# Kernel tuning notes

Hardware: AMD Instinct MI355X
Metric: run time of the kernel (lower is better)

Reference implementation:

```python
import jax, jax.numpy as jnp
import numpy as np

B, H, L, D = 8, 16, 1024, 64


def setup_inputs() -> dict:
    key = jax.random.key(0)
    kq, kk, kv, kb, km = jax.random.split(key, 5)
    q = jax.random.normal(kq, (B, H, L, D), dtype=jnp.float32)
    k = jax.random.normal(kk, (B, H, L, D), dtype=jnp.float32)
    v = jax.random.normal(kv, (B, H, L, D), dtype=jnp.float32)
    # relative-position bias, broadcast over batch
    bias = jax.random.normal(kb, (1, H, L, L), dtype=jnp.float32)
    # variable-length padding mask: each sequence has length in [L//2, L]
    lengths = jax.random.randint(km, (B,), L // 2, L + 1)
    mask = jnp.arange(L)[None, :] < lengths[:, None]  # [B, L] bool
    return {"q": q, "k": k, "v": v, "mask": mask, "bias": bias}


def reference(q, k, v, mask, bias):
    # dots: [b h m n]; NOTE: source computes self.scale but never applies it
    dots = jnp.einsum('bhmd,bhnd->bhmn', q, k) + bias
    # mask[:, None, None, :] & mask[:, None, :, None]
    m2 = mask[:, None, None, :] & mask[:, None, :, None]  # [b 1 m n]
    neg = jnp.finfo(dots.dtype).min
    probs = jax.nn.softmax(jnp.where(m2, dots, neg), axis=-1)
    probs = jnp.where(m2, probs, jnp.zeros((), dtype=probs.dtype))  # XSoftmax zeroing
    # dropout is identity in eval mode
    context = jnp.einsum('bhmn,bhnd->bhmd', probs, v)
    b, h, m, d = context.shape
    return context.transpose(0, 2, 1, 3).reshape(b, m, h * d)  # [b m (h d)]
```

## Files before the change

kernel.cpp:

```cpp
#include <hip/hip_runtime.h>
#include <hip/hip_bf16.h>

#define B_ 8
#define H_ 16
#define L_ 1024
#define D_ 64

typedef __attribute__((ext_vector_type(8))) short short8;
typedef __attribute__((ext_vector_type(4))) short short4v;
typedef __attribute__((ext_vector_type(4))) float floatx4;

__device__ inline short bf16s(float f) {
    union { float f; unsigned u; } un; un.f = f;
    unsigned u = un.u;
    u += 0x7FFFu + ((u >> 16) & 1u);
    return (short)(u >> 16);
}
__device__ inline float bf16f(unsigned short u) {
    union { unsigned u; float f; } un; un.u = ((unsigned)u) << 16;
    return un.f;
}

__device__ inline floatx4 mfma16(short8 a, short8 b, floatx4 c) {
    return __builtin_amdgcn_mfma_f32_16x16x32_bf16(a, b, c, 0, 0, 0);
}

#define KSTR 72
#define VSTR 40
#define PSTR 40
#define KPL (32 * KSTR)
#define VPL (64 * VSTR)
#define PPL (16 * PSTR)

__launch_bounds__(256, 4)
__global__ void prep_kernel(const float* __restrict__ k,
                            const float* __restrict__ v,
                            unsigned short* __restrict__ khi,
                            unsigned short* __restrict__ klo,
                            unsigned short* __restrict__ vth) {
    __shared__ alignas(16) short vt[64 * 72];
    const int bid = blockIdx.x;
    const int kt  = bid & 15;
    const int h   = (bid >> 4) & 15;
    const int b   = bid >> 8;
    const int tid = threadIdx.x;
    const size_t base = ((size_t)(b * H_ + h) * L_ + kt * 64) * D_;

    #pragma unroll
    for (int i = 0; i < 4; i++) {
        const int idx = (i * 256 + tid) * 4;
        const float4 f = *(const float4*)(k + base + idx);
        short4v hi, lo;
        hi[0] = bf16s(f.x); lo[0] = bf16s(f.x - bf16f((unsigned short)hi[0]));
        hi[1] = bf16s(f.y); lo[1] = bf16s(f.y - bf16f((unsigned short)hi[1]));
        hi[2] = bf16s(f.z); lo[2] = bf16s(f.z - bf16f((unsigned short)hi[2]));
        hi[3] = bf16s(f.w); lo[3] = bf16s(f.w - bf16f((unsigned short)hi[3]));
        *(short4v*)(khi + base + idx) = hi;
        *(short4v*)(klo + base + idx) = lo;
    }

    #pragma unroll
    for (int i = 0; i < 4; i++) {
        const int idx = (i * 256 + tid) * 4;
        const int key = idx >> 6;
        const int d0  = idx & 63;
        const float4 f = *(const float4*)(v + base + idx);
        vt[(d0 + 0) * 72 + key] = bf16s(f.x);
        vt[(d0 + 1) * 72 + key] = bf16s(f.y);
        vt[(d0 + 2) * 72 + key] = bf16s(f.z);
        vt[(d0 + 3) * 72 + key] = bf16s(f.w);
    }
    __syncthreads();
    #pragma unroll
    for (int i = 0; i < 2; i++) {
        const int s = i * 2048 + tid * 8;
        const int d = s >> 6;
        const int kk = s & 63;
        short8 r = *(const short8*)&vt[d * 72 + kk];
        *(short8*)(vth + ((size_t)((b * H_ + h) * D_) + d) * L_ + kt * 64 + kk) = r;
    }
}

__launch_bounds__(256, 4)
__global__ void attn_fast(const float* __restrict__ q,
                          const unsigned short* __restrict__ khi,
                          const unsigned short* __restrict__ klo,
                          const unsigned short* __restrict__ vth,
                          const void* __restrict__ mask,
                          const float* __restrict__ bias,
                          float* __restrict__ out) {
    __shared__ alignas(16) short lds_k[2 * 2 * KPL];
    __shared__ alignas(16) short lds_vt[2 * VPL];
    __shared__ alignas(16) short lds_p[4 * 2 * PPL];
    __shared__ int s_len;

    const int bid  = blockIdx.x;
    const int b    = (bid >> 3) & 7;
    const int p_   = ((bid >> 6) << 3) | (bid & 7);
    const int h    = p_ >> 4;
    const int mt   = p_ & 15;
    const int tid  = threadIdx.x;
    const int wave = tid >> 6;
    const int lane = tid & 63;
    const int l16  = lane & 15;
    const int quad = lane >> 4;
    short* lds_pw = lds_p + wave * (2 * PPL);

    if (tid == 0) s_len = 0;
    __syncthreads();
    {
        const unsigned char* mb = (const unsigned char*)mask;
        int fmt;
        if (mb[0] == 1 && mb[1] != 0)      fmt = 0;
        else if (mb[0] == 1)               fmt = 1;
        else if (mb[1] != 0)               fmt = 2;
        else                               fmt = 1;
        int s = 0;
        if (fmt == 0) {
            const unsigned char* r = mb + b * L_;
            #pragma unroll
            for (int i = 0; i < 4; i++) s += (r[tid * 4 + i] != 0);
        } else if (fmt == 1) {
            const unsigned int* r = (const unsigned int*)mask + b * L_;
            #pragma unroll
            for (int i = 0; i < 4; i++) s += (r[tid * 4 + i] != 0u);
        } else {
            const unsigned short* r = (const unsigned short*)mask + b * L_;
            #pragma unroll
            for (int i = 0; i < 4; i++) s += (r[tid * 4 + i] != 0);
        }
        #pragma unroll
        for (int off = 32; off; off >>= 1) s += __shfl_down(s, off);
        if (lane == 0) atomicAdd(&s_len, s);
    }
    __syncthreads();
    const int len = s_len;

    const int m_base = mt * 64 + wave * 16;
    const float* qp = q + ((size_t)((b * H_ + h) * L_) + (m_base + l16)) * D_;
    short8 qh[2], ql[2];
    #pragma unroll
    for (int c = 0; c < 2; c++)
        #pragma unroll
        for (int j = 0; j < 8; j++) {
            float x = qp[c * 32 + quad * 8 + j];
            short hh = bf16s(x);
            qh[c][j] = hh;
            ql[c][j] = bf16s(x - bf16f((unsigned short)hh));
        }

    floatx4 acc[4];
    float l_p[4];
    #pragma unroll
    for (int c = 0; c < 4; c++) { acc[c][0] = acc[c][1] = acc[c][2] = acc[c][3] = 0.f; }
    #pragma unroll
    for (int r = 0; r < 4; r++) l_p[r] = 0.f;

    const size_t kvoff = (size_t)((b * H_ + h) * L_) * D_;
    const size_t vtoff = (size_t)((b * H_ + h) * D_) * L_;
    const float* bias_base = bias + (size_t)h * L_ * L_
                           + (size_t)(m_base + quad * 4) * L_ + l16;

    const int ntiles = (len + 31) >> 5;

    const int key_s = tid >> 3;
    const int d_s   = (tid & 7) * 8;
    const int dv    = tid >> 2;
    const int k8v   = (tid & 3) * 8;

    short8 kh_r, kl_r, vv_r;
    float bc[8], bn[8];

    short8 pf_prev;
    short8 vfr0, vfr1, vfr2, vfr3;

    {
        const size_t ksrc = kvoff + (size_t)tid * 8;
        kh_r = *(const short8*)(khi + ksrc);
        kl_r = *(const short8*)(klo + ksrc);
        vv_r = *(const short8*)(vth + vtoff + (size_t)dv * L_ + k8v);
        #pragma unroll
        for (int r = 0; r < 4; r++) {
            bc[2 * r]     = bias_base[(size_t)r * L_];
            bc[2 * r + 1] = bias_base[(size_t)r * L_ + 16];
        }
        *(short8*)&lds_k[key_s * KSTR + d_s] = kh_r;
        *(short8*)&lds_k[KPL + key_s * KSTR + d_s] = kl_r;
        *(short8*)&lds_vt[dv * VSTR + k8v] = vv_r;
    }
    __syncthreads();

    for (int kt = 0; kt < ntiles; kt++) {
        const int n0 = kt * 32;
        short* kb = lds_k + (kt & 1) * (2 * KPL);
        short* vb = lds_vt + (kt & 1) * VPL;
        short* pw = lds_pw + (kt & 1) * PPL;
        const bool pfetch = (kt + 1 < ntiles);

        if (kt > 0) {
            __builtin_amdgcn_s_setprio(1);
            acc[0] = mfma16(pf_prev, vfr0, acc[0]);
            acc[1] = mfma16(pf_prev, vfr1, acc[1]);
            acc[2] = mfma16(pf_prev, vfr2, acc[2]);
            acc[3] = mfma16(pf_prev, vfr3, acc[3]);
            __builtin_amdgcn_s_setprio(0);
        }

        if (pfetch) {
            const size_t ksrc = kvoff + (size_t)(n0 + 32) * D_ + (size_t)tid * 8;
            kh_r = *(const short8*)(khi + ksrc);
            kl_r = *(const short8*)(klo + ksrc);
            vv_r = *(const short8*)(vth + vtoff + (size_t)dv * L_ + (n0 + 32) + k8v);
            #pragma unroll
            for (int r = 0; r < 4; r++) {
                bn[2 * r]     = bias_base[(size_t)r * L_ + n0 + 32];
                bn[2 * r + 1] = bias_base[(size_t)r * L_ + n0 + 48];
            }
        }

        vfr0 = *(const short8*)&vb[(0 * 16 + l16) * VSTR + quad * 8];
        vfr1 = *(const short8*)&vb[(1 * 16 + l16) * VSTR + quad * 8];
        vfr2 = *(const short8*)&vb[(2 * 16 + l16) * VSTR + quad * 8];
        vfr3 = *(const short8*)&vb[(3 * 16 + l16) * VSTR + quad * 8];

        floatx4 s0, s1;
        s0[0]=s0[1]=s0[2]=s0[3]=0.f;
        s1[0]=s1[1]=s1[2]=s1[3]=0.f;
        __builtin_amdgcn_s_setprio(1);
        #pragma unroll
        for (int c = 0; c < 2; c++) {
            const int o0 = l16 * KSTR + c * 32 + quad * 8;
            const int o1 = (16 + l16) * KSTR + c * 32 + quad * 8;
            short8 k0h = *(const short8*)&kb[o0];
            short8 k1h = *(const short8*)&kb[o1];
            short8 k0l = *(const short8*)&kb[KPL + o0];
            short8 k1l = *(const short8*)&kb[KPL + o1];
            s0 = mfma16(qh[c], k0h, s0);
            s0 = mfma16(ql[c], k0h, s0);
            s0 = mfma16(qh[c], k0l, s0);
            s1 = mfma16(qh[c], k1h, s1);
            s1 = mfma16(ql[c], k1h, s1);
            s1 = mfma16(qh[c], k1l, s1);
        }
        __builtin_amdgcn_s_setprio(0);

        #pragma unroll
        for (int r = 0; r < 4; r++) { s0[r] += bc[2 * r]; s1[r] += bc[2 * r + 1]; }
        if (n0 + l16      >= len) { s0[0]=s0[1]=s0[2]=s0[3] = -1e30f; }
        if (n0 + 16 + l16 >= len) { s1[0]=s1[1]=s1[2]=s1[3] = -1e30f; }

        #pragma unroll
        for (int r = 0; r < 4; r++) {
            const float p0 = __expf(fminf(s0[r], 60.f));
            const float p1 = __expf(fminf(s1[r], 60.f));
            l_p[r] += p0 + p1;
            const int row = quad * 4 + r;
            pw[row * PSTR + l16]      = bf16s(p0);
            pw[row * PSTR + 16 + l16] = bf16s(p1);
        }

        pf_prev = *(const short8*)&pw[l16 * PSTR + quad * 8];

        if (pfetch) {
            short* kb2 = lds_k + ((kt + 1) & 1) * (2 * KPL);
            short* vb2 = lds_vt + ((kt + 1) & 1) * VPL;
            *(short8*)&kb2[key_s * KSTR + d_s] = kh_r;
            *(short8*)&kb2[KPL + key_s * KSTR + d_s] = kl_r;
            *(short8*)&vb2[dv * VSTR + k8v] = vv_r;
            #pragma unroll
            for (int i = 0; i < 8; i++) bc[i] = bn[i];
        }
        __syncthreads();
    }

    {
        __builtin_amdgcn_s_setprio(1);
        acc[0] = mfma16(pf_prev, vfr0, acc[0]);
        acc[1] = mfma16(pf_prev, vfr1, acc[1]);
        acc[2] = mfma16(pf_prev, vfr2, acc[2]);
        acc[3] = mfma16(pf_prev, vfr3, acc[3]);
        __builtin_amdgcn_s_setprio(0);
    }

    #pragma unroll
    for (int r = 0; r < 4; r++) {
        float ls = l_p[r];
        #pragma unroll
        for (int off = 8; off; off >>= 1) ls += __shfl_xor(ls, off);
        const int mg = m_base + quad * 4 + r;
        const bool valid = (mg < len);
        const float invl = (ls > 0.f) ? (1.0f / ls) : 0.f;
        float* op = out + (size_t)(b * L_ + mg) * (H_ * D_) + h * D_;
        #pragma unroll
        for (int c = 0; c < 4; c++)
            op[c * 16 + l16] = valid ? acc[c][r] * invl : 0.f;
    }
}

__launch_bounds__(256, 4)
__global__ void attn_fallback(const float* __restrict__ q,
                              const float* __restrict__ k,
                              const float* __restrict__ v,
                              const void* __restrict__ mask,
                              const float* __restrict__ bias,
                              float* __restrict__ out) {
    __shared__ alignas(16) short lds_k[2 * KPL];
    __shared__ alignas(16) short lds_vt[2 * VPL];
    __shared__ alignas(16) short lds_p[4 * 2 * PPL];
    __shared__ int s_len;

    const int bid  = blockIdx.x;
    const int mt   = bid & 15;
    const int h    = (bid >> 4) & 15;
    const int b    = bid >> 8;
    const int tid  = threadIdx.x;
    const int wave = tid >> 6;
    const int lane = tid & 63;
    const int l16  = lane & 15;
    const int quad = lane >> 4;
    short* lds_pw = lds_p + wave * (2 * PPL);

    if (tid == 0) s_len = 0;
    __syncthreads();
    {
        const unsigned char* mb = (const unsigned char*)mask;
        int fmt;
        if (mb[0] == 1 && mb[1] != 0)      fmt = 0;
        else if (mb[0] == 1)               fmt = 1;
        else if (mb[1] != 0)               fmt = 2;
        else                               fmt = 1;
        int s = 0;
        if (fmt == 0) {
            const unsigned char* r = mb + b * L_;
            for (int i = 0; i < 4; i++) s += (r[tid * 4 + i] != 0);
        } else if (fmt == 1) {
            const unsigned int* r = (const unsigned int*)mask + b * L_;
            for (int i = 0; i < 4; i++) s += (r[tid * 4 + i] != 0u);
        } else {
            const unsigned short* r = (const unsigned short*)mask + b * L_;
            for (int i = 0; i < 4; i++) s += (r[tid * 4 + i] != 0);
        }
        for (int off = 32; off; off >>= 1) s += __shfl_down(s, off);
        if (lane == 0) atomicAdd(&s_len, s);
    }
    __syncthreads();
    const int len = s_len;

    const int m_base = mt * 64 + wave * 16;
    const float* qp = q + ((size_t)((b * H_ + h) * L_) + (m_base + l16)) * D_;
    short8 qh[2], ql[2];
    for (int c = 0; c < 2; c++)
        for (int j = 0; j < 8; j++) {
            float x = qp[c * 32 + quad * 8 + j];
            short hh = bf16s(x);
            qh[c][j] = hh;
            ql[c][j] = bf16s(x - bf16f((unsigned short)hh));
        }

    floatx4 acc[4];
    float m_i[4], l_i[4];
    for (int c = 0; c < 4; c++) { acc[c][0]=acc[c][1]=acc[c][2]=acc[c][3]=0.f; }
    for (int r = 0; r < 4; r++) { m_i[r] = -1e30f; l_i[r] = 0.f; }

    const size_t kvoff = (size_t)((b * H_ + h) * L_) * D_;
    const size_t boff0 = (size_t)h * L_ * L_;
    const int ntiles = (len + 31) >> 5;

    for (int kt = 0; kt < ntiles; kt++) {
        const int n0 = kt * 32;
        __syncthreads();
        {
            const int e0  = tid * 8;
            const int key = e0 >> 6;
            const int d0  = e0 & 63;
            const float* ksrc = k + kvoff + (size_t)(n0 + key) * D_ + d0;
            const float* vsrc = v + kvoff + (size_t)(n0 + key) * D_ + d0;
            short* kdh = &lds_k[key * KSTR + d0];
            for (int i = 0; i < 8; i++) {
                float x = ksrc[i];
                short hh = bf16s(x);
                kdh[i]       = hh;
                kdh[KPL + i] = bf16s(x - bf16f((unsigned short)hh));
            }
            for (int i = 0; i < 8; i++) {
                float x = vsrc[i];
                short hh = bf16s(x);
                lds_vt[(d0 + i) * VSTR + key]       = hh;
                lds_vt[VPL + (d0 + i) * VSTR + key] = bf16s(x - bf16f((unsigned short)hh));
            }
        }
        __syncthreads();

        floatx4 s0, s1;
        s0[0]=s0[1]=s0[2]=s0[3]=0.f;
        s1[0]=s1[1]=s1[2]=s1[3]=0.f;
        for (int c = 0; c < 2; c++) {
            const int o0 = l16 * KSTR + c * 32 + quad * 8;
            const int o1 = (16 + l16) * KSTR + c * 32 + quad * 8;
            short8 k0h = *(const short8*)&lds_k[o0];
            short8 k1h = *(const short8*)&lds_k[o1];
            short8 k0l = *(const short8*)&lds_k[KPL + o0];
            short8 k1l = *(const short8*)&lds_k[KPL + o1];
            s0 = mfma16(qh[c], k0h, s0);
            s0 = mfma16(ql[c], k0h, s0);
            s0 = mfma16(qh[c], k0l, s0);
            s1 = mfma16(qh[c], k1h, s1);
            s1 = mfma16(ql[c], k1h, s1);
            s1 = mfma16(qh[c], k1l, s1);
        }

        for (int r = 0; r < 4; r++) {
            const float* bp = bias + boff0 + (size_t)(m_base + quad * 4 + r) * L_ + n0;
            s0[r] += bp[l16];
            s1[r] += bp[16 + l16];
        }
        if (n0 + l16      >= len) { s0[0]=s0[1]=s0[2]=s0[3] = -1e30f; }
        if (n0 + 16 + l16 >= len) { s1[0]=s1[1]=s1[2]=s1[3] = -1e30f; }

        for (int r = 0; r < 4; r++) {
            float mx = fmaxf(s0[r], s1[r]);
            for (int off = 8; off; off >>= 1) mx = fmaxf(mx, __shfl_xor(mx, off));
            const float mnew  = fmaxf(m_i[r], mx);
            const float alpha = __expf(m_i[r] - mnew);
            const float p0 = __expf(s0[r] - mnew);
            const float p1 = __expf(s1[r] - mnew);
            float ps = p0 + p1;
            for (int off = 8; off; off >>= 1) ps += __shfl_xor(ps, off);
            l_i[r] = l_i[r] * alpha + ps;
            m_i[r] = mnew;
            for (int c = 0; c < 4; c++) acc[c][r] *= alpha;
            const int row = quad * 4 + r;
            short h0 = bf16s(p0), h1 = bf16s(p1);
            lds_pw[row * PSTR + l16]      = h0;
            lds_pw[row * PSTR + 16 + l16] = h1;
            lds_pw[PPL + row * PSTR + l16]      = bf16s(p0 - bf16f((unsigned short)h0));
            lds_pw[PPL + row * PSTR + 16 + l16] = bf16s(p1 - bf16f((unsigned short)h1));
        }

        short8 pfh = *(const short8*)&lds_pw[l16 * PSTR + quad * 8];
        short8 pfl = *(const short8*)&lds_pw[PPL + l16 * PSTR + quad * 8];
        for (int c = 0; c < 4; c++) {
            const int vo = (c * 16 + l16) * VSTR + quad * 8;
            short8 vfh = *(const short8*)&lds_vt[vo];
            short8 vfl = *(const short8*)&lds_vt[VPL + vo];
            acc[c] = mfma16(pfh, vfh, acc[c]);
            acc[c] = mfma16(pfl, vfh, acc[c]);
            acc[c] = mfma16(pfh, vfl, acc[c]);
        }
    }

    for (int r = 0; r < 4; r++) {
        const int mg = m_base + quad * 4 + r;
        const bool valid = (mg < len);
        const float invl = (l_i[r] > 0.f) ? (1.0f / l_i[r]) : 0.f;
        float* op = out + (size_t)(b * L_ + mg) * (H_ * D_) + h * D_;
        for (int c = 0; c < 4; c++)
            op[c * 16 + l16] = valid ? acc[c][r] * invl : 0.f;
    }
}

extern "C" void kernel_launch(void* const* d_in, const int* in_sizes, int n_in,
                              void* d_out, int out_size, void* d_ws, size_t ws_size,
                              hipStream_t stream) {
    const float* q    = (const float*)d_in[0];
    const float* k    = (const float*)d_in[1];
    const float* v    = (const float*)d_in[2];
    const void*  mask = d_in[3];
    const float* bias = (const float*)d_in[4];
    float* out = (float*)d_out;

    const size_t PLANE = (size_t)B_ * H_ * L_ * D_;
    const size_t need  = 3 * PLANE * sizeof(unsigned short);

    dim3 grid(B_ * H_ * (L_ / 64));
    if (ws_size >= need) {
        unsigned short* khi = (unsigned short*)d_ws;
        unsigned short* klo = khi + PLANE;
        unsigned short* vth = klo + PLANE;
        prep_kernel<<<grid, 256, 0, stream>>>(k, v, khi, klo, vth);
        attn_fast<<<grid, 256, 0, stream>>>(q, khi, klo, vth, mask, bias, out);
    } else {
        attn_fallback<<<grid, 256, 0, stream>>>(q, k, v, mask, bias, out);
    }
}
```

Measured before the change: 270.1 us.

## Compute transposed QK^T to keep P in registers and drop LDS round trip

Swaps the MFMA operand order so the score tile comes out transposed, with each lane holding consecutive key columns for one query row. With a permuted key-row layout in LDS, the bf16 probabilities can be packed directly into the A operand of the PV MFMA, removing the per-wave LDS write/read of P and its shared buffer. Bias loads become two vectorized float4 loads per row, and the row-sum reduction moves to a final cross-quad shuffle. The risk is that the key permutation and the accumulator lane mapping must match exactly, or the output is silently wrong.

```diff
diff --git a/kernel.cpp b/kernel.cpp
--- a/kernel.cpp
+++ b/kernel.cpp
@@ -91,7 +91,6 @@
                           float* __restrict__ out) {
     __shared__ alignas(16) short lds_k[2 * 2 * KPL];
     __shared__ alignas(16) short lds_vt[2 * VPL];
-    __shared__ alignas(16) short lds_p[4 * 2 * PPL];
     __shared__ int s_len;
 
     const int bid  = blockIdx.x;
@@ -104,7 +103,6 @@
     const int lane = tid & 63;
     const int l16  = lane & 15;
     const int quad = lane >> 4;
-    short* lds_pw = lds_p + wave * (2 * PPL);
 
     if (tid == 0) s_len = 0;
     __syncthreads();
@@ -150,26 +148,25 @@
         }
 
     floatx4 acc[4];
-    float l_p[4];
+    float l_p = 0.f;
     #pragma unroll
     for (int c = 0; c < 4; c++) { acc[c][0] = acc[c][1] = acc[c][2] = acc[c][3] = 0.f; }
-    #pragma unroll
-    for (int r = 0; r < 4; r++) l_p[r] = 0.f;
 
     const size_t kvoff = (size_t)((b * H_ + h) * L_) * D_;
     const size_t vtoff = (size_t)((b * H_ + h) * D_) * L_;
-    const float* bias_base = bias + (size_t)h * L_ * L_
-                           + (size_t)(m_base + quad * 4) * L_ + l16;
+    const float* bias_row = bias + (size_t)h * L_ * L_
+                          + (size_t)(m_base + l16) * L_ + quad * 8;
 
     const int ntiles = (len + 31) >> 5;
 
     const int key_s = tid >> 3;
+    const int rperm = ((key_s >> 3) << 2) + (key_s & 3) + ((key_s & 4) << 2);
     const int d_s   = (tid & 7) * 8;
     const int dv    = tid >> 2;
     const int k8v   = (tid & 3) * 8;
 
     short8 kh_r, kl_r, vv_r;
-    float bc[8], bn[8];
+    floatx4 bc0, bc1, bn0, bn1;
 
     short8 pf_prev;
     short8 vfr0, vfr1, vfr2, vfr3;
@@ -179,13 +176,10 @@
         kh_r = *(const short8*)(khi + ksrc);
         kl_r = *(const short8*)(klo + ksrc);
         vv_r = *(const short8*)(vth + vtoff + (size_t)dv * L_ + k8v);
-        #pragma unroll
-        for (int r = 0; r < 4; r++) {
-            bc[2 * r]     = bias_base[(size_t)r * L_];
-            bc[2 * r + 1] = bias_base[(size_t)r * L_ + 16];
-        }
-        *(short8*)&lds_k[key_s * KSTR + d_s] = kh_r;
-        *(short8*)&lds_k[KPL + key_s * KSTR + d_s] = kl_r;
+        bc0 = *(const floatx4*)(bias_row + 0);
+        bc1 = *(const floatx4*)(bias_row + 4);
+        *(short8*)&lds_k[rperm * KSTR + d_s] = kh_r;
+        *(short8*)&lds_k[KPL + rperm * KSTR + d_s] = kl_r;
         *(short8*)&lds_vt[dv * VSTR + k8v] = vv_r;
     }
     __syncthreads();
@@ -194,7 +188,6 @@
         const int n0 = kt * 32;
         short* kb = lds_k + (kt & 1) * (2 * KPL);
         short* vb = lds_vt + (kt & 1) * VPL;
-        short* pw = lds_pw + (kt & 1) * PPL;
         const bool pfetch = (kt + 1 < ntiles);
 
         if (kt > 0) {
@@ -211,11 +204,8 @@
             kh_r = *(const short8*)(khi + ksrc);
             kl_r = *(const short8*)(klo + ksrc);
             vv_r = *(const short8*)(vth + vtoff + (size_t)dv * L_ + (n0 + 32) + k8v);
-            #pragma unroll
-            for (int r = 0; r < 4; r++) {
-                bn[2 * r]     = bias_base[(size_t)r * L_ + n0 + 32];
-                bn[2 * r + 1] = bias_base[(size_t)r * L_ + n0 + 48];
-            }
+            bn0 = *(const floatx4*)(bias_row + n0 + 32);
+            bn1 = *(const floatx4*)(bias_row + n0 + 36);
         }
 
         vfr0 = *(const short8*)&vb[(0 * 16 + l16) * VSTR + quad * 8];
@@ -235,40 +225,46 @@
             short8 k1h = *(const short8*)&kb[o1];
             short8 k0l = *(const short8*)&kb[KPL + o0];
             short8 k1l = *(const short8*)&kb[KPL + o1];
-            s0 = mfma16(qh[c], k0h, s0);
-            s0 = mfma16(ql[c], k0h, s0);
-            s0 = mfma16(qh[c], k0l, s0);
-            s1 = mfma16(qh[c], k1h, s1);
-            s1 = mfma16(ql[c], k1h, s1);
-            s1 = mfma16(qh[c], k1l, s1);
+            s0 = mfma16(k0h, qh[c], s0);
+            s0 = mfma16(k0h, ql[c], s0);
+            s0 = mfma16(k0l, qh[c], s0);
+            s1 = mfma16(k1h, qh[c], s1);
+            s1 = mfma16(k1h, ql[c], s1);
+            s1 = mfma16(k1l, qh[c], s1);
         }
         __builtin_amdgcn_s_setprio(0);
 
         #pragma unroll
-        for (int r = 0; r < 4; r++) { s0[r] += bc[2 * r]; s1[r] += bc[2 * r + 1]; }
-        if (n0 + l16      >= len) { s0[0]=s0[1]=s0[2]=s0[3] = -1e30f; }
-        if (n0 + 16 + l16 >= len) { s1[0]=s1[1]=s1[2]=s1[3] = -1e30f; }
-
+        for (int r = 0; r < 4; r++) { s0[r] += bc0[r]; s1[r] += bc1[r]; }
+        if (n0 + 32 > len) {
+            #pragma unroll
+            for (int r = 0; r < 4; r++) {
+                if (n0 + quad * 8 + r     >= len) s0[r] = -1e30f;
+                if (n0 + quad * 8 + 4 + r >= len) s1[r] = -1e30f;
+            }
+        }
+
+        float p0[4], p1[4];
         #pragma unroll
         for (int r = 0; r < 4; r++) {
-            const float p0 = __expf(fminf(s0[r], 60.f));
-            const float p1 = __expf(fminf(s1[r], 60.f));
-            l_p[r] += p0 + p1;
-            const int row = quad * 4 + r;
-            pw[row * PSTR + l16]      = bf16s(p0);
-            pw[row * PSTR + 16 + l16] = bf16s(p1);
-        }
-
-        pf_prev = *(const short8*)&pw[l16 * PSTR + quad * 8];
+            p0[r] = __expf(fminf(s0[r], 60.f));
+            p1[r] = __expf(fminf(s1[r], 60.f));
+        }
+        l_p += ((p0[0] + p0[1]) + (p0[2] + p0[3]))
+             + ((p1[0] + p1[1]) + (p1[2] + p1[3]));
+        #pragma unroll
+        for (int r = 0; r < 4; r++) {
+            pf_prev[r]     = bf16s(p0[r]);
+            pf_prev[4 + r] = bf16s(p1[r]);
+        }
 
         if (pfetch) {
             short* kb2 = lds_k + ((kt + 1) & 1) * (2 * KPL);
             short* vb2 = lds_vt + ((kt + 1) & 1) * VPL;
-            *(short8*)&kb2[key_s * KSTR + d_s] = kh_r;
-            *(short8*)&kb2[KPL + key_s * KSTR + d_s] = kl_r;
+            *(short8*)&kb2[rperm * KSTR + d_s] = kh_r;
+            *(short8*)&kb2[KPL + rperm * KSTR + d_s] = kl_r;
             *(short8*)&vb2[dv * VSTR + k8v] = vv_r;
-            #pragma unroll
-            for (int i = 0; i < 8; i++) bc[i] = bn[i];
+            bc0 = bn0; bc1 = bn1;
         }
         __syncthreads();
     }
@@ -282,14 +278,15 @@
         __builtin_amdgcn_s_setprio(0);
     }
 
+    float ls = l_p;
+    ls += __shfl_xor(ls, 16);
+    ls += __shfl_xor(ls, 32);
     #pragma unroll
     for (int r = 0; r < 4; r++) {
-        float ls = l_p[r];
-        #pragma unroll
-        for (int off = 8; off; off >>= 1) ls += __shfl_xor(ls, off);
+        const float lsr = __shfl(ls, quad * 4 + r);
         const int mg = m_base + quad * 4 + r;
         const bool valid = (mg < len);
-        const float invl = (ls > 0.f) ? (1.0f / ls) : 0.f;
+        const float invl = (lsr > 0.f) ? (1.0f / lsr) : 0.f;
         float* op = out + (size_t)(b * L_ + mg) * (H_ * D_) + h * D_;
         #pragma unroll
         for (int c = 0; c < 4; c++)
```

Result: slower. 280.7 us (+3.9%).
